# Kernel tuning notes

Hardware: AMD Instinct MI355X
Metric: run time of the kernel (lower is better)

## Reference

```python
import jax, jax.numpy as jnp
import numpy as np

EPS = 1e-5
N_KNN = 16


def _knn_idx(query_feat, ref_feat, k):
    # query_feat: (B, N, C), ref_feat: (B, M, C) -> idx (B, N, k) of smallest sq-dist
    q2 = jnp.sum(query_feat * query_feat, axis=-1, keepdims=True)        # (B,N,1)
    r2 = jnp.sum(ref_feat * ref_feat, axis=-1)[:, None, :]               # (B,1,M)
    d = q2 + r2 - 2.0 * jnp.einsum('bnc,bmc->bnm', query_feat, ref_feat)  # (B,N,M)
    _, idx = jax.lax.top_k(-d, k)
    return idx


def _group(x, idx):
    # x: (B, C, M), idx: (B, N, k) -> (B, C, N, k)
    B, C, M = x.shape
    _, N, k = idx.shape
    flat = jnp.broadcast_to(idx.reshape(B, 1, N * k), (B, C, N * k))
    return jnp.take_along_axis(x, flat, axis=2).reshape(B, C, N, k)


def _bn(x, g, b, m, v):
    # eval-mode BatchNorm2d over channel axis 1 of (B,C,N,k)
    inv = g / jnp.sqrt(v + EPS)
    return x * inv[None, :, None, None] + (b - m * inv)[None, :, None, None]


def setup_inputs() -> dict:
    key = jax.random.key(0)
    ks = jax.random.split(key, 24)
    B, C, N, N2 = 4, 256, 2048, 2048
    ph = 64  # pos_hidden_dim
    ah = 256  # dim * attn_hidden_multiplier = 64*4
    s = lambda fan: 1.0 / np.sqrt(fan)
    inp = {
        'pcd': jax.random.normal(ks[0], (B, 3, N), jnp.float32),
        'feat': jax.random.normal(ks[1], (B, C, N), jnp.float32),
        'pcd_feadb': jax.random.normal(ks[2], (B, 3, N2), jnp.float32),
        'feat_feadb': jax.random.normal(ks[3], (B, C, N2), jnp.float32),
        'pos_w1': jax.random.normal(ks[4], (ph, 3), jnp.float32) * s(3),
        'pos_b1': jax.random.normal(ks[5], (ph,), jnp.float32) * 0.01,
        'pos_g': jax.random.uniform(ks[6], (ph,), jnp.float32, 0.5, 1.5),
        'pos_be': jax.random.normal(ks[7], (ph,), jnp.float32) * 0.01,
        'pos_m': jax.random.normal(ks[8], (ph,), jnp.float32) * 0.1,
        'pos_v': jax.random.uniform(ks[9], (ph,), jnp.float32, 0.5, 1.5),
        'pos_w2': jax.random.normal(ks[10], (C, ph), jnp.float32) * s(ph),
        'pos_b2': jax.random.normal(ks[11], (C,), jnp.float32) * 0.01,
        'attn_w1': jax.random.normal(ks[12], (ah, C), jnp.float32) * s(C),
        'attn_b1': jax.random.normal(ks[13], (ah,), jnp.float32) * 0.01,
        'attn_g': jax.random.uniform(ks[14], (ah,), jnp.float32, 0.5, 1.5),
        'attn_be': jax.random.normal(ks[15], (ah,), jnp.float32) * 0.01,
        'attn_m': jax.random.normal(ks[16], (ah,), jnp.float32) * 0.1,
        'attn_v': jax.random.uniform(ks[17], (ah,), jnp.float32, 0.5, 1.5),
        'attn_w2': jax.random.normal(ks[18], (C, ah), jnp.float32) * s(ah),
        'attn_b2': jax.random.normal(ks[19], (C,), jnp.float32) * 0.01,
    }
    return inp


def reference(pcd, feat, pcd_feadb, feat_feadb,
              pos_w1, pos_b1, pos_g, pos_be, pos_m, pos_v, pos_w2, pos_b2,
              attn_w1, attn_b1, attn_g, attn_be, attn_m, attn_v, attn_w2, attn_b2):
    fusion_pcd = jnp.concatenate([pcd, pcd_feadb], axis=2)    # (B,3,M)
    fusion_feat = jnp.concatenate([feat, feat_feadb], axis=2)  # (B,C,M)
    # KNN in feature space: neighbors of each key point among fusion set
    idx = _knn_idx(jnp.swapaxes(feat, 1, 2), jnp.swapaxes(fusion_feat, 1, 2), N_KNN)  # (B,N,k)
    group_point = _group(fusion_pcd, idx)   # (B,3,N,k)
    group_feat = _group(fusion_feat, idx)   # (B,C,N,k)
    qk_rel = feat[:, :, :, None] - group_feat
    pos_rel = pcd[:, :, :, None] - group_point
    # pos_mlp: conv1x1 -> BN -> relu -> conv1x1
    h = jnp.einsum('oc,bcnk->bonk', pos_w1, pos_rel) + pos_b1[None, :, None, None]
    h = jax.nn.relu(_bn(h, pos_g, pos_be, pos_m, pos_v))
    pos_embedding = jnp.einsum('oc,bcnk->bonk', pos_w2, h) + pos_b2[None, :, None, None]
    # attn_mlp
    a = jnp.einsum('oc,bcnk->bonk', attn_w1, qk_rel + pos_embedding) + attn_b1[None, :, None, None]
    a = jax.nn.relu(_bn(a, attn_g, attn_be, attn_m, attn_v))
    a = jnp.einsum('oc,bcnk->bonk', attn_w2, a) + attn_b2[None, :, None, None]
    sample_weight = jax.nn.softmax(a, axis=-1)  # softmax over the k neighbors
    refined_feat = jnp.sum(sample_weight * (group_feat + pos_embedding), axis=-1)  # (B,C,N)
    return refined_feat
```

## Files before the change

### kernel.cpp

```cpp
#include <hip/hip_runtime.h>
#include <float.h>

#define CDIM 256
#define NPTS 2048
#define MPTS 4096
#define NB   4
#define KNN  16
#define COLS 64
#define NCHUNK 8
#define CSIZE  512
#define NSTEPS 16

typedef _Float16 half8 __attribute__((ext_vector_type(8)));
typedef _Float16 half4 __attribute__((ext_vector_type(4)));
typedef float    f32x4 __attribute__((ext_vector_type(4)));

__device__ __forceinline__ int swzS(int row, int byte) {
    return row * 512 + (byte ^ ((row & 7) << 4));
}
__device__ __forceinline__ int swz128(int row, int byte) {
    return row * 128 + (byte ^ ((row & 7) << 4));
}

__device__ __forceinline__ float sum16(float v) {
    v += __uint_as_float(__builtin_amdgcn_update_dpp(0, __float_as_uint(v), 0x128, 0xF, 0xF, true));
    v += __uint_as_float(__builtin_amdgcn_update_dpp(0, __float_as_uint(v), 0x124, 0xF, 0xF, true));
    v += __uint_as_float(__builtin_amdgcn_update_dpp(0, __float_as_uint(v), 0x122, 0xF, 0xF, true));
    v += __uint_as_float(__builtin_amdgcn_update_dpp(0, __float_as_uint(v), 0x121, 0xF, 0xF, true));
    return v;
}

#define CEA(x, y)                                                               \
    { unsigned lo_ = kk[x] < kk[y] ? kk[x] : kk[y];                             \
      unsigned hi_ = kk[x] < kk[y] ? kk[y] : kk[x];                             \
      kk[x] = lo_; kk[y] = hi_; }
#define CED(x, y)                                                               \
    { unsigned hi_ = td[x] > td[y] ? td[x] : td[y];                             \
      unsigned lo_ = td[x] > td[y] ? td[y] : td[x];                             \
      td[x] = hi_; td[y] = lo_; }
#define RESORT16                                                                \
    CED(0,8) CED(1,9) CED(2,10) CED(3,11) CED(4,12) CED(5,13) CED(6,14) CED(7,15) \
    CED(0,4) CED(1,5) CED(2,6) CED(3,7) CED(8,12) CED(9,13) CED(10,14) CED(11,15) \
    CED(0,2) CED(1,3) CED(4,6) CED(5,7) CED(8,10) CED(9,11) CED(12,14) CED(13,15) \
    CED(0,1) CED(2,3) CED(4,5) CED(6,7) CED(8,9) CED(10,11) CED(12,13) CED(14,15)

__global__ __launch_bounds__(256) void tposeHL2(const float* __restrict__ feat,
                                                const float* __restrict__ featdb,
                                                _Float16* __restrict__ featH,
                                                _Float16* __restrict__ featL,
                                                float* __restrict__ r2) {
    __shared__ float red[8][33];
    const int b = blockIdx.y;
    const int mt = blockIdx.x;
    const int m = threadIdx.x & 31;
    const int cp = threadIdx.x >> 5;
    const int mg = mt * 32 + m;
    const float* src = (mg < NPTS) ? (feat + (size_t)b * CDIM * NPTS + mg)
                                   : (featdb + (size_t)b * CDIM * NPTS + (mg - NPTS));
    const int c0 = cp * 32;
    float acc = 0.f;
    half8 hh[4], ll[4];
#pragma unroll
    for (int i = 0; i < 32; i++) {
        float v = src[(size_t)(c0 + i) * NPTS];
        acc += v * v;
        _Float16 h = (_Float16)v;
        hh[i >> 3][i & 7] = h;
        ll[i >> 3][i & 7] = (_Float16)(v - (float)h);
    }
    _Float16* dh = featH + ((size_t)b * MPTS + mg) * CDIM + c0;
    _Float16* dl = featL + ((size_t)b * MPTS + mg) * CDIM + c0;
#pragma unroll
    for (int i = 0; i < 4; i++) {
        *(half8*)(dh + i * 8) = hh[i];
        *(half8*)(dl + i * 8) = ll[i];
    }
    red[cp][m] = acc;
    __syncthreads();
    if (threadIdx.x < 32) {
        float s = 0.f;
#pragma unroll
        for (int j = 0; j < 8; j++) s += red[j][threadIdx.x];
        r2[b * MPTS + mt * 32 + threadIdx.x] = s;
    }
}

__global__ __launch_bounds__(256) void wcvt(const float* __restrict__ aw1,
                                            const float* __restrict__ aw2,
                                            const float* __restrict__ pw2,
                                            _Float16* __restrict__ aw1h,
                                            _Float16* __restrict__ aw2h,
                                            _Float16* __restrict__ pw2h) {
    int i = blockIdx.x * 256 + threadIdx.x;
    if (i < 65536) { aw1h[i] = (_Float16)aw1[i]; aw2h[i] = (_Float16)aw2[i]; }
    if (i < 16384) { pw2h[i] = (_Float16)pw2[i]; }
}

__global__ __launch_bounds__(256) void score_knn(const _Float16* __restrict__ featH,
                                                 const _Float16* __restrict__ featL,
                                                 const float* __restrict__ r2g,
                                                 unsigned* __restrict__ partial) {
    __shared__ __align__(16) char sbuf[65536];
    __shared__ float sr2[CSIZE];

    const int tid = threadIdx.x;
    const int lane = tid & 63, wave = tid >> 6;
    const int l15 = lane & 15, l4 = lane >> 4;
    const int chunk = blockIdx.x, qt = blockIdx.y, b = blockIdx.z;
    const int nq = qt * 64 + wave * 16 + l15;
    const int m0 = chunk * CSIZE;

    for (int i = tid; i < CSIZE; i += 256) sr2[i] = r2g[b * MPTS + m0 + i];

    half8 qh[8], ql[8];
    {
        const _Float16* qb = featH + ((size_t)b * MPTS + nq) * CDIM + l4 * 8;
        const _Float16* qL = featL + ((size_t)b * MPTS + nq) * CDIM + l4 * 8;
#pragma unroll
        for (int ks = 0; ks < 8; ks++) {
            qh[ks] = *(const half8*)(qb + ks * 32);
            ql[ks] = *(const half8*)(qL + ks * 32);
        }
    }

    int adr[8];
#pragma unroll
    for (int ks = 0; ks < 8; ks++)
        adr[ks] = (ks * 4 + l4) * 512 + ((l15 * 16) ^ ((ks & 7) << 4));

    int wadr[4];
#pragma unroll
    for (int j = 0; j < 4; j++)
        wadr[j] = ((tid & 7) * 4 + j) * 512 + (((tid >> 3) * 16) ^ ((tid & 7) << 4));
    const char* gH = (const char*)(featH + ((size_t)b * MPTS + m0 + (tid >> 3)) * CDIM) +
                     (tid & 7) * 64;
    const char* gL = (const char*)(featL + ((size_t)b * MPTS + m0 + (tid >> 3)) * CDIM) +
                     (tid & 7) * 64;

    unsigned td[16];
#pragma unroll
    for (int i = 0; i < 16; i++) td[i] = 0xFFFFFFFFu;

    half8 pH[4], pL[4];
#pragma unroll
    for (int j = 0; j < 4; j++) {
        pH[j] = *(const half8*)(gH + j * 16);
        pL[j] = *(const half8*)(gL + j * 16);
    }
    gH += 32 * CDIM * 2;
    gL += 32 * CDIM * 2;

    for (int s = 0; s < NSTEPS; ++s) {
        char* buf = sbuf + (s & 1) * 32768;
#pragma unroll
        for (int j = 0; j < 4; j++) {
            *(half8*)(buf + wadr[j])         = pH[j];
            *(half8*)(buf + 16384 + wadr[j]) = pL[j];
        }
        __syncthreads();

        if (s < NSTEPS - 1) {
#pragma unroll
            for (int j = 0; j < 4; j++) {
                pH[j] = *(const half8*)(gH + j * 16);
                pL[j] = *(const half8*)(gL + j * 16);
            }
            gH += 32 * CDIM * 2;
            gL += 32 * CDIM * 2;
        }

        unsigned kk[8];
#pragma unroll
        for (int sub = 0; sub < 2; ++sub) {
            f32x4 a0 = {0.f, 0.f, 0.f, 0.f};
            f32x4 a1 = {0.f, 0.f, 0.f, 0.f};
            f32x4 a2 = {0.f, 0.f, 0.f, 0.f};
#pragma unroll
            for (int ks = 0; ks < 8; ks++) {
                half8 ah = *(const half8*)(buf + adr[ks] + sub * 256);
                half8 al = *(const half8*)(buf + 16384 + adr[ks] + sub * 256);
                a0 = __builtin_amdgcn_mfma_f32_16x16x32_f16(ah, qh[ks], a0, 0, 0, 0);
                a1 = __builtin_amdgcn_mfma_f32_16x16x32_f16(ah, ql[ks], a1, 0, 0, 0);
                a2 = __builtin_amdgcn_mfma_f32_16x16x32_f16(al, qh[ks], a2, 0, 0, 0);
            }
            float4 s4 = *(const float4*)(sr2 + s * 32 + sub * 16 + 4 * l4);
            const float sv[4] = {s4.x, s4.y, s4.z, s4.w};
            const int mloc0 = s * 32 + sub * 16 + 4 * l4;
#pragma unroll
            for (int r = 0; r < 4; r++) {
                float d = fmaxf(sv[r] - 2.f * (a0[r] + a1[r] + a2[r]), 0.f);
                unsigned dq = (unsigned)(d * 4096.f);
                dq = dq > 0x7FFFF0u ? 0x7FFFF0u : dq;
                kk[sub * 4 + r] = (dq << 9) | (unsigned)(mloc0 + r);
            }
        }
        CEA(0,1) CEA(2,3) CEA(4,5) CEA(6,7)
        CEA(0,2) CEA(1,3) CEA(4,6) CEA(5,7)
        CEA(1,2) CEA(5,6) CEA(0,4) CEA(3,7)
        CEA(1,5) CEA(2,6)
        CEA(1,4) CEA(3,6)
        CEA(2,4) CEA(3,5)
        CEA(3,4)
#pragma unroll
        for (int i = 0; i < 8; i++) td[i] = td[i] < kk[i] ? td[i] : kk[i];
        RESORT16
    }

#pragma unroll
    for (int rr = 0; rr < 2; rr++) {
        const int dx = 16 << rr;
        unsigned ot[16];
#pragma unroll
        for (int e = 0; e < 16; e++) ot[e] = __shfl_xor(td[e], dx);
#pragma unroll
        for (int e = 0; e < 16; e++) {
            unsigned o = ot[15 - e];
            td[e] = td[e] < o ? td[e] : o;
        }
        RESORT16
    }
    if (l4 == 0) {
        const size_t qrow = (size_t)b * NPTS + qt * 64 + wave * 16 + l15;
#pragma unroll
        for (int e = 0; e < 16; e++)
            partial[(size_t)(chunk * 16 + e) * (NB * NPTS) + qrow] = td[e];
    }
}

__global__ __launch_bounds__(256) void merge16(const unsigned* __restrict__ partial,
                                               int* __restrict__ idxout) {
    const int row = blockIdx.x * 256 + threadIdx.x;
    unsigned long long td[16];
#pragma unroll
    for (int i = 0; i < 16; i++) td[i] = 0x8000000000ull + (unsigned long long)i;
    unsigned long long curmax = 0x800000000Full;
    for (int e = 0; e < NCHUNK * 16; e++) {
        unsigned k = partial[(size_t)e * (NB * NPTS) + row];
        unsigned long long k64 =
            (((unsigned long long)(k >> 9)) << 12) |
            (unsigned long long)((unsigned)((e >> 4) << 9) | (k & 0x1FFu));
        if (k64 < curmax) {
#pragma unroll
            for (int i_ = 0; i_ < 16; i_++) td[i_] = (td[i_] == curmax) ? k64 : td[i_];
            unsigned long long nm_ = td[0];
#pragma unroll
            for (int i_ = 1; i_ < 16; i_++) nm_ = td[i_] > nm_ ? td[i_] : nm_;
            curmax = nm_;
        }
    }
#pragma unroll
    for (int e = 0; e < 16; e++) idxout[row * 16 + e] = (int)(td[e] & 0xFFFull);
}

__global__ __launch_bounds__(512, 4) void fused_mlp6(
    const float* __restrict__ pcd, const float* __restrict__ pcddb,
    const _Float16* __restrict__ featH, const int* __restrict__ knn,
    const float* __restrict__ pw1, const float* __restrict__ pb1,
    const float* __restrict__ pg, const float* __restrict__ pbe,
    const float* __restrict__ pm, const float* __restrict__ pv,
    const _Float16* __restrict__ pw2h, const float* __restrict__ pb2,
    const _Float16* __restrict__ aw1h, const float* __restrict__ ab1,
    const float* __restrict__ ag, const float* __restrict__ abe,
    const float* __restrict__ am, const float* __restrict__ av,
    const _Float16* __restrict__ aw2h,
    float* __restrict__ out) {
    __shared__ __align__(16) _Float16 xbuf[COLS * 256];
    __shared__ __align__(16) _Float16 hbuf[COLS * 64];
    __shared__ __align__(16) float pr[3][COLS];
    __shared__ int sidx[COLS];
    __shared__ __align__(16) float ainv[256], ash2[256], pinv[64], psh[64];

    const int tid = threadIdx.x;
    const int lane = tid & 63, wave = tid >> 6;
    const int l15 = lane & 15, l4 = lane >> 4;
    const int blk = blockIdx.x;
    const int b = blk >> 9;
    const int n0 = (blk & 511) * 4;
    const int R0 = wave * 32;

    if (tid < COLS) {
        sidx[tid] = knn[(size_t)(b * NPTS + n0 + (tid >> 4)) * KNN + (tid & 15)];
    } else if (tid < COLS + 256) {
        int c = tid - COLS;
        float inv = ag[c] / sqrtf(av[c] + 1e-5f);
        ainv[c] = inv;
        ash2[c] = abe[c] - am[c] * inv + ab1[c] * inv;
    } else if (tid < COLS + 256 + 64) {
        int o = tid - COLS - 256;
        float inv = pg[o] / sqrtf(pv[o] + 1e-5f);
        pinv[o] = inv;
        psh[o] = pbe[o] - pm[o] * inv;
    }
    half8 wp[2][2];
#pragma unroll
    for (int rt = 0; rt < 2; rt++)
#pragma unroll
        for (int ks = 0; ks < 2; ks++)
            wp[rt][ks] = *(const half8*)(pw2h + (size_t)(R0 + rt * 16 + l15) * 64 +
                                         ks * 32 + l4 * 8);
    __syncthreads();

    if (tid < 3 * COLS) {
        int c = tid >> 6, col = tid & 63;
        int m = sidx[col];
        const float* pc = pcd + ((size_t)b * 3 + c) * NPTS;
        const float* px = pcddb + ((size_t)b * 3 + c) * NPTS;
        float gp = (m < NPTS) ? pc[m] : px[m - NPTS];
        pr[c][col] = pc[n0 + (col >> 4)] - gp;
    }
    const int colx = tid & 63;
    const int c0x = (tid >> 6) * 32;
    half8 fmv[4], fnv[4];
    {
        const _Float16* fmp = featH + ((size_t)b * MPTS + sidx[colx]) * CDIM + c0x;
        const _Float16* fnp = featH + ((size_t)b * MPTS + n0 + (colx >> 4)) * CDIM + c0x;
#pragma unroll
        for (int j = 0; j < 4; j++) {
            fmv[j] = *(const half8*)(fmp + j * 8);
            fnv[j] = *(const half8*)(fnp + j * 8);
        }
    }
    __syncthreads();

    {
        int col = tid >> 3, o0 = (tid & 7) * 8;
        float x0 = pr[0][col], x1 = pr[1][col], x2 = pr[2][col];
        half8 hv;
#pragma unroll
        for (int i = 0; i < 8; i++) {
            int o = o0 + i;
            float v = pw1[o * 3] * x0 + pw1[o * 3 + 1] * x1 + pw1[o * 3 + 2] * x2 + pb1[o];
            v = fmaxf(v * pinv[o] + psh[o], 0.f);
            hv[i] = (_Float16)v;
        }
        *(half8*)((char*)hbuf + swz128(col, o0 * 2)) = hv;
    }
    __syncthreads();

    f32x4 acc[2][4];
#pragma unroll
    for (int rt = 0; rt < 2; rt++)
#pragma unroll
        for (int ct = 0; ct < 4; ct++) acc[rt][ct] = (f32x4){0.f, 0.f, 0.f, 0.f};
#pragma unroll
    for (int ks = 0; ks < 2; ks++) {
        int k0 = ks * 32 + l4 * 8;
#pragma unroll
        for (int ct = 0; ct < 4; ct++) {
            half8 bb = *(const half8*)((char*)hbuf + swz128(ct * 16 + l15, k0 * 2));
            acc[0][ct] = __builtin_amdgcn_mfma_f32_16x16x32_f16(wp[0][ks], bb, acc[0][ct], 0, 0, 0);
            acc[1][ct] = __builtin_amdgcn_mfma_f32_16x16x32_f16(wp[1][ks], bb, acc[1][ct], 0, 0, 0);
        }
    }
    half4 pe4[2][4];
#pragma unroll
    for (int rt = 0; rt < 2; rt++) {
        int cb = R0 + rt * 16 + 4 * l4;
        float4 pb = *(const float4*)(pb2 + cb);
        float pbv[4] = {pb.x, pb.y, pb.z, pb.w};
#pragma unroll
        for (int ct = 0; ct < 4; ct++) {
            int col = ct * 16 + l15;
            half4 p4;
#pragma unroll
            for (int r = 0; r < 4; r++) p4[r] = (_Float16)(acc[rt][ct][r] + pbv[r]);
            pe4[rt][ct] = p4;
            *(half4*)((char*)xbuf + swzS(col, cb * 2)) = p4;
        }
    }
    __syncthreads();

#pragma unroll
    for (int j = 0; j < 4; j++) {
        int c = c0x + j * 8;
        half8 vp = *(const half8*)((char*)xbuf + swzS(colx, c * 2));
        half8 xv = fnv[j] - fmv[j] + vp;
        *(half8*)((char*)xbuf + swzS(colx, c * 2)) = xv;
    }
    half8 wa[8];
#pragma unroll
    for (int ks = 0; ks < 8; ks++)
        wa[ks] = *(const half8*)(aw1h + (size_t)(R0 + l15) * 256 + ks * 32 + l4 * 8);
    __syncthreads();

#pragma unroll
    for (int rt = 0; rt < 2; rt++)
#pragma unroll
        for (int ct = 0; ct < 4; ct++) acc[rt][ct] = (f32x4){0.f, 0.f, 0.f, 0.f};
#pragma unroll
    for (int ks = 0; ks < 8; ks++) {
        int k0 = ks * 32 + l4 * 8;
#pragma unroll
        for (int ct = 0; ct < 4; ct++) {
            half8 bb = *(const half8*)((char*)xbuf + swzS(ct * 16 + l15, k0 * 2));
            acc[0][ct] = __builtin_amdgcn_mfma_f32_16x16x32_f16(wa[ks], bb, acc[0][ct], 0, 0, 0);
        }
    }
#pragma unroll
    for (int ks = 0; ks < 8; ks++)
        wa[ks] = *(const half8*)(aw1h + (size_t)(R0 + 16 + l15) * 256 + ks * 32 + l4 * 8);
#pragma unroll
    for (int ks = 0; ks < 8; ks++) {
        int k0 = ks * 32 + l4 * 8;
#pragma unroll
        for (int ct = 0; ct < 4; ct++) {
            half8 bb = *(const half8*)((char*)xbuf + swzS(ct * 16 + l15, k0 * 2));
            acc[1][ct] = __builtin_amdgcn_mfma_f32_16x16x32_f16(wa[ks], bb, acc[1][ct], 0, 0, 0);
        }
    }
    __syncthreads();

#pragma unroll
    for (int rt = 0; rt < 2; rt++) {
        int cb = R0 + rt * 16 + 4 * l4;
        float4 iv = *(const float4*)(&ainv[cb]);
        float4 sh = *(const float4*)(&ash2[cb]);
        float ivv[4] = {iv.x, iv.y, iv.z, iv.w};
        float shv[4] = {sh.x, sh.y, sh.z, sh.w};
#pragma unroll
        for (int ct = 0; ct < 4; ct++) {
            int col = ct * 16 + l15;
            half4 h4;
#pragma unroll
            for (int r = 0; r < 4; r++)
                h4[r] = (_Float16)fmaxf(acc[rt][ct][r] * ivv[r] + shv[r], 0.f);
            *(half4*)((char*)xbuf + swzS(col, cb * 2)) = h4;
        }
    }
#pragma unroll
    for (int ks = 0; ks < 8; ks++)
        wa[ks] = *(const half8*)(aw2h + (size_t)(R0 + l15) * 256 + ks * 32 + l4 * 8);
    __syncthreads();

#pragma unroll
    for (int rt = 0; rt < 2; rt++)
#pragma unroll
        for (int ct = 0; ct < 4; ct++) acc[rt][ct] = (f32x4){0.f, 0.f, 0.f, 0.f};
#pragma unroll
    for (int ks = 0; ks < 8; ks++) {
        int k0 = ks * 32 + l4 * 8;
#pragma unroll
        for (int ct = 0; ct < 4; ct++) {
            half8 bb = *(const half8*)((char*)xbuf + swzS(ct * 16 + l15, k0 * 2));
            acc[0][ct] = __builtin_amdgcn_mfma_f32_16x16x32_f16(wa[ks], bb, acc[0][ct], 0, 0, 0);
        }
    }
#pragma unroll
    for (int ks = 0; ks < 8; ks++)
        wa[ks] = *(const half8*)(aw2h + (size_t)(R0 + 16 + l15) * 256 + ks * 32 + l4 * 8);
#pragma unroll
    for (int ks = 0; ks < 8; ks++) {
        int k0 = ks * 32 + l4 * 8;
#pragma unroll
        for (int ct = 0; ct < 4; ct++) {
            half8 bb = *(const half8*)((char*)xbuf + swzS(ct * 16 + l15, k0 * 2));
            acc[1][ct] = __builtin_amdgcn_mfma_f32_16x16x32_f16(wa[ks], bb, acc[1][ct], 0, 0, 0);
        }
    }

#pragma unroll
    for (int rt = 0; rt < 2; rt++) {
        int cb = R0 + rt * 16 + 4 * l4;
        half4 gfa[4];
#pragma unroll
        for (int ct = 0; ct < 4; ct++)
            gfa[ct] = *(const half4*)(featH +
                ((size_t)b * MPTS + sidx[ct * 16 + l15]) * CDIM + cb);
#pragma unroll
        for (int ct = 0; ct < 4; ct++) {
            float oo[4], ss[4];
#pragma unroll
            for (int r = 0; r < 4; r++) {
                float v = acc[rt][ct][r];
                v = fminf(fmaxf(v, -60.f), 60.f);
                float e = __expf(v);
                float sv = (float)gfa[ct][r] + (float)pe4[rt][ct][r];
                ss[r] = sum16(e);
                oo[r] = sum16(e * sv);
            }
            if (l15 < 4) {
                float o = l15 == 0 ? oo[0] : l15 == 1 ? oo[1] : l15 == 2 ? oo[2] : oo[3];
                float s = l15 == 0 ? ss[0] : l15 == 1 ? ss[1] : l15 == 2 ? ss[2] : ss[3];
                out[((size_t)b * CDIM + cb + l15) * NPTS + n0 + ct] =
                    o * __builtin_amdgcn_rcpf(s);
            }
        }
    }
}

extern "C" void kernel_launch(void* const* d_in, const int* in_sizes, int n_in,
                              void* d_out, int out_size, void* d_ws, size_t ws_size,
                              hipStream_t stream) {
    const float* pcd    = (const float*)d_in[0];
    const float* feat   = (const float*)d_in[1];
    const float* pcddb  = (const float*)d_in[2];
    const float* featdb = (const float*)d_in[3];
    const float* pw1 = (const float*)d_in[4];
    const float* pb1 = (const float*)d_in[5];
    const float* pg  = (const float*)d_in[6];
    const float* pbe = (const float*)d_in[7];
    const float* pm  = (const float*)d_in[8];
    const float* pv  = (const float*)d_in[9];
    const float* pw2 = (const float*)d_in[10];
    const float* pb2 = (const float*)d_in[11];
    const float* aw1 = (const float*)d_in[12];
    const float* ab1 = (const float*)d_in[13];
    const float* ag  = (const float*)d_in[14];
    const float* abe = (const float*)d_in[15];
    const float* am  = (const float*)d_in[16];
    const float* av  = (const float*)d_in[17];
    const float* aw2 = (const float*)d_in[18];
    float* out = (float*)d_out;

    char* ws = (char*)d_ws;
    _Float16* featH   = (_Float16*)(ws);
    _Float16* featL   = (_Float16*)(ws + 8388608);
    float*    ws_r2   = (float*)(ws + 16777216);
    unsigned* partial = (unsigned*)(ws + 16842752);
    int*      ws_idx  = (int*)(ws + 21037056);
    _Float16* aw1h    = (_Float16*)(ws + 21561344);
    _Float16* aw2h    = (_Float16*)(ws + 21692416);
    _Float16* pw2h    = (_Float16*)(ws + 21823488);

    wcvt<<<256, 256, 0, stream>>>(aw1, aw2, pw2, aw1h, aw2h, pw2h);
    tposeHL2<<<dim3(MPTS / 32, NB), 256, 0, stream>>>(feat, featdb, featH, featL, ws_r2);
    score_knn<<<dim3(NCHUNK, NPTS / 64, NB), 256, 0, stream>>>(featH, featL, ws_r2, partial);
    merge16<<<NB * NPTS / 256, 256, 0, stream>>>(partial, ws_idx);
    fused_mlp6<<<NB * (NPTS / 4), 512, 0, stream>>>(
        pcd, pcddb, featH, ws_idx,
        pw1, pb1, pg, pbe, pm, pv, pw2h, pb2,
        aw1h, ab1, ag, abe, am, av, aw2h, out);
}
```

Measured before the change: 275.1 us.

## Double queries per KNN block and fold gather into MLP register layout

```diff
diff --git a/kernel.cpp b/kernel.cpp
--- a/kernel.cpp
+++ b/kernel.cpp
@@ -10,6 +10,7 @@
 #define NCHUNK 8
 #define CSIZE  512
 #define NSTEPS 16
+#define QPB   128
 
 typedef _Float16 half8 __attribute__((ext_vector_type(8)));
 typedef _Float16 half4 __attribute__((ext_vector_type(4)));
@@ -96,10 +97,10 @@
     if (i < 16384) { pw2h[i] = (_Float16)pw2[i]; }
 }
 
-__global__ __launch_bounds__(256) void score_knn(const _Float16* __restrict__ featH,
-                                                 const _Float16* __restrict__ featL,
-                                                 const float* __restrict__ r2g,
-                                                 unsigned* __restrict__ partial) {
+__global__ __launch_bounds__(512, 4) void score_knn(const _Float16* __restrict__ featH,
+                                                    const _Float16* __restrict__ featL,
+                                                    const float* __restrict__ r2g,
+                                                    unsigned* __restrict__ partial) {
     __shared__ __align__(16) char sbuf[65536];
     __shared__ float sr2[CSIZE];
 
@@ -107,10 +108,10 @@
     const int lane = tid & 63, wave = tid >> 6;
     const int l15 = lane & 15, l4 = lane >> 4;
     const int chunk = blockIdx.x, qt = blockIdx.y, b = blockIdx.z;
-    const int nq = qt * 64 + wave * 16 + l15;
+    const int nq = qt * QPB + wave * 16 + l15;
     const int m0 = chunk * CSIZE;
 
-    for (int i = tid; i < CSIZE; i += 256) sr2[i] = r2g[b * MPTS + m0 + i];
+    sr2[tid] = r2g[b * MPTS + m0 + tid];
 
     half8 qh[8], ql[8];
     {
@@ -128,22 +129,24 @@
     for (int ks = 0; ks < 8; ks++)
         adr[ks] = (ks * 4 + l4) * 512 + ((l15 * 16) ^ ((ks & 7) << 4));
 
-    int wadr[4];
-#pragma unroll
-    for (int j = 0; j < 4; j++)
-        wadr[j] = ((tid & 7) * 4 + j) * 512 + (((tid >> 3) * 16) ^ ((tid & 7) << 4));
-    const char* gH = (const char*)(featH + ((size_t)b * MPTS + m0 + (tid >> 3)) * CDIM) +
-                     (tid & 7) * 64;
-    const char* gL = (const char*)(featL + ((size_t)b * MPTS + m0 + (tid >> 3)) * CDIM) +
-                     (tid & 7) * 64;
+    const int srow = tid >> 4;
+    const int o0 = 2 * (tid & 15);
+    int wadr[2];
+#pragma unroll
+    for (int j = 0; j < 2; j++) {
+        int o = o0 + j;
+        wadr[j] = o * 512 + ((srow * 16) ^ (((o >> 2) & 7) << 4));
+    }
+    const char* gH = (const char*)(featH + ((size_t)b * MPTS + m0 + srow) * CDIM) + o0 * 16;
+    const char* gL = (const char*)(featL + ((size_t)b * MPTS + m0 + srow) * CDIM) + o0 * 16;
 
     unsigned td[16];
 #pragma unroll
     for (int i = 0; i < 16; i++) td[i] = 0xFFFFFFFFu;
 
-    half8 pH[4], pL[4];
-#pragma unroll
-    for (int j = 0; j < 4; j++) {
+    half8 pH[2], pL[2];
+#pragma unroll
+    for (int j = 0; j < 2; j++) {
         pH[j] = *(const half8*)(gH + j * 16);
         pL[j] = *(const half8*)(gL + j * 16);
     }
@@ -153,7 +156,7 @@
     for (int s = 0; s < NSTEPS; ++s) {
         char* buf = sbuf + (s & 1) * 32768;
 #pragma unroll
-        for (int j = 0; j < 4; j++) {
+        for (int j = 0; j < 2; j++) {
             *(half8*)(buf + wadr[j])         = pH[j];
             *(half8*)(buf + 16384 + wadr[j]) = pL[j];
         }
@@ -161,7 +164,7 @@
 
         if (s < NSTEPS - 1) {
 #pragma unroll
-            for (int j = 0; j < 4; j++) {
+            for (int j = 0; j < 2; j++) {
                 pH[j] = *(const half8*)(gH + j * 16);
                 pL[j] = *(const half8*)(gL + j * 16);
             }
@@ -220,7 +223,7 @@
         RESORT16
     }
     if (l4 == 0) {
-        const size_t qrow = (size_t)b * NPTS + qt * 64 + wave * 16 + l15;
+        const size_t qrow = (size_t)b * NPTS + qt * QPB + wave * 16 + l15;
 #pragma unroll
         for (int e = 0; e < 16; e++)
             partial[(size_t)(chunk * 16 + e) * (NB * NPTS) + qrow] = td[e];
@@ -252,7 +255,7 @@
     for (int e = 0; e < 16; e++) idxout[row * 16 + e] = (int)(td[e] & 0xFFFull);
 }
 
-__global__ __launch_bounds__(512, 4) void fused_mlp6(
+__global__ __launch_bounds__(512, 4) void fused_mlp7(
     const float* __restrict__ pcd, const float* __restrict__ pcddb,
     const _Float16* __restrict__ featH, const int* __restrict__ knn,
     const float* __restrict__ pw1, const float* __restrict__ pb1,
@@ -264,8 +267,9 @@
     const float* __restrict__ am, const float* __restrict__ av,
     const _Float16* __restrict__ aw2h,
     float* __restrict__ out) {
-    __shared__ __align__(16) _Float16 xbuf[COLS * 256];
-    __shared__ __align__(16) _Float16 hbuf[COLS * 64];
+    __shared__ __align__(16) char smem[COLS * 256 * 2];
+    _Float16* xbuf = (_Float16*)smem;
+    _Float16* hbuf = (_Float16*)smem;
     __shared__ __align__(16) float pr[3][COLS];
     __shared__ int sidx[COLS];
     __shared__ __align__(16) float ainv[256], ash2[256], pinv[64], psh[64];
@@ -308,18 +312,6 @@
         float gp = (m < NPTS) ? pc[m] : px[m - NPTS];
         pr[c][col] = pc[n0 + (col >> 4)] - gp;
     }
-    const int colx = tid & 63;
-    const int c0x = (tid >> 6) * 32;
-    half8 fmv[4], fnv[4];
-    {
-        const _Float16* fmp = featH + ((size_t)b * MPTS + sidx[colx]) * CDIM + c0x;
-        const _Float16* fnp = featH + ((size_t)b * MPTS + n0 + (colx >> 4)) * CDIM + c0x;
-#pragma unroll
-        for (int j = 0; j < 4; j++) {
-            fmv[j] = *(const half8*)(fmp + j * 8);
-            fnv[j] = *(const half8*)(fnp + j * 8);
-        }
-    }
     __syncthreads();
 
     {
@@ -360,22 +352,27 @@
         float pbv[4] = {pb.x, pb.y, pb.z, pb.w};
 #pragma unroll
         for (int ct = 0; ct < 4; ct++) {
-            int col = ct * 16 + l15;
             half4 p4;
 #pragma unroll
             for (int r = 0; r < 4; r++) p4[r] = (_Float16)(acc[rt][ct][r] + pbv[r]);
             pe4[rt][ct] = p4;
-            *(half4*)((char*)xbuf + swzS(col, cb * 2)) = p4;
-        }
-    }
-    __syncthreads();
-
-#pragma unroll
-    for (int j = 0; j < 4; j++) {
-        int c = c0x + j * 8;
-        half8 vp = *(const half8*)((char*)xbuf + swzS(colx, c * 2));
-        half8 xv = fnv[j] - fmv[j] + vp;
-        *(half8*)((char*)xbuf + swzS(colx, c * 2)) = xv;
+        }
+    }
+    __syncthreads();
+
+    half4 fm4[2][4];
+#pragma unroll
+    for (int rt = 0; rt < 2; rt++) {
+        int cb = R0 + rt * 16 + 4 * l4;
+#pragma unroll
+        for (int ct = 0; ct < 4; ct++) {
+            int col = ct * 16 + l15;
+            half4 fn4 = *(const half4*)(featH + ((size_t)b * MPTS + n0 + ct) * CDIM + cb);
+            half4 fm = *(const half4*)(featH + ((size_t)b * MPTS + sidx[col]) * CDIM + cb);
+            fm4[rt][ct] = fm;
+            half4 xv = fn4 - fm + pe4[rt][ct];
+            *(half4*)((char*)xbuf + swzS(col, cb * 2)) = xv;
+        }
     }
     half8 wa[8];
 #pragma unroll
@@ -461,11 +458,6 @@
 #pragma unroll
     for (int rt = 0; rt < 2; rt++) {
         int cb = R0 + rt * 16 + 4 * l4;
-        half4 gfa[4];
-#pragma unroll
-        for (int ct = 0; ct < 4; ct++)
-            gfa[ct] = *(const half4*)(featH +
-                ((size_t)b * MPTS + sidx[ct * 16 + l15]) * CDIM + cb);
 #pragma unroll
         for (int ct = 0; ct < 4; ct++) {
             float oo[4], ss[4];
@@ -474,7 +466,7 @@
                 float v = acc[rt][ct][r];
                 v = fminf(fmaxf(v, -60.f), 60.f);
                 float e = __expf(v);
-                float sv = (float)gfa[ct][r] + (float)pe4[rt][ct][r];
+                float sv = (float)fm4[rt][ct][r] + (float)pe4[rt][ct][r];
                 ss[r] = sum16(e);
                 oo[r] = sum16(e * sv);
             }
@@ -524,9 +516,9 @@
 
     wcvt<<<256, 256, 0, stream>>>(aw1, aw2, pw2, aw1h, aw2h, pw2h);
     tposeHL2<<<dim3(MPTS / 32, NB), 256, 0, stream>>>(feat, featdb, featH, featL, ws_r2);
-    score_knn<<<dim3(NCHUNK, NPTS / 64, NB), 256, 0, stream>>>(featH, featL, ws_r2, partial);
+    score_knn<<<dim3(NCHUNK, NPTS / QPB, NB), 512, 0, stream>>>(featH, featL, ws_r2, partial);
     merge16<<<NB * NPTS / 256, 256, 0, stream>>>(partial, ws_idx);
-    fused_mlp6<<<NB * (NPTS / 4), 512, 0, stream>>>(
+    fused_mlp7<<<NB * (NPTS / 4), 512, 0, stream>>>(
         pcd, pcddb, featH, ws_idx,
         pw1, pb1, pg, pbe, pm, pv, pw2h, pb2,
         aw1h, ab1, ag, abe, am, av, aw2h, out);
```

Result: no change. 280.0 us (+1.8%).
